# Optimization experiments

Hardware: AMD Instinct MI355X
Metric: run time of the kernel (lower is better)

## Reference

```python
import jax, jax.numpy as jnp
import numpy as np

DIM = 1024
NUM_HEADS = 16
HEAD_DIM = DIM // NUM_HEADS
ROPE_BASE = 10000.0


def _rope_cache(seq_len, head_dim, dtype=jnp.float32):
    inv_freq = 1.0 / (ROPE_BASE ** (jnp.arange(0, head_dim, 2, dtype=jnp.float32) / head_dim))
    t = jnp.arange(seq_len, dtype=jnp.float32)
    freqs = jnp.einsum('i,j->ij', t, inv_freq)          # [S, hd/2]
    emb = jnp.concatenate([freqs, freqs], axis=-1)       # [S, hd]
    return jnp.cos(emb).astype(dtype), jnp.sin(emb).astype(dtype)


def _rotate_half(x):
    x1, x2 = jnp.split(x, 2, axis=-1)
    return jnp.concatenate([-x2, x1], axis=-1)


def setup_inputs() -> dict:
    key = jax.random.key(0)
    k1, k2, k3 = jax.random.split(key, 3)
    B, S, D = 2, 2048, DIM
    x = jax.random.normal(k1, (B, S, D), dtype=jnp.float32)
    mask = jnp.tril(jnp.ones((S, S), dtype=jnp.bool_))   # causal mask
    w_qkv = jax.random.normal(k2, (D, 3 * D), dtype=jnp.float32) * (D ** -0.5)
    w_out = jax.random.normal(k3, (D, D), dtype=jnp.float32) * (D ** -0.5)
    return {"x": x, "w_qkv": w_qkv, "w_out": w_out, "mask": mask}


def reference(x, w_qkv, w_out, mask):
    B, S, D = x.shape
    H, hd = NUM_HEADS, HEAD_DIM
    qkv = x @ w_qkv                                       # [B,S,3D]
    q, k, v = jnp.split(qkv, 3, axis=-1)
    # [B,H,S,hd]
    q = q.reshape(B, S, H, hd).transpose(0, 2, 1, 3)
    k = k.reshape(B, S, H, hd).transpose(0, 2, 1, 3)
    v = v.reshape(B, S, H, hd).transpose(0, 2, 1, 3)
    cos, sin = _rope_cache(S, hd, q.dtype)               # [S,hd]
    q = q * cos + _rotate_half(q) * sin
    k = k * cos + _rotate_half(k) * sin
    scale = hd ** -0.5
    scores = jnp.einsum('bhqd,bhkd->bhqk', q, k) * scale  # [B,H,S,S]
    neg = jnp.finfo(scores.dtype).min
    scores = jnp.where(mask[None, None, :, :], scores, neg)
    attn = jax.nn.softmax(scores, axis=-1)                # dropout off (eval)
    out = jnp.einsum('bhqk,bhkd->bhqd', attn, v)
    out = out.transpose(0, 2, 1, 3).reshape(B, S, D)
    return out @ w_out
```

## Files before the change

kernel.cpp:

```cpp
#include <hip/hip_runtime.h>

typedef __attribute__((ext_vector_type(8))) short short8;
typedef __attribute__((ext_vector_type(4))) float f32x4;
typedef __attribute__((ext_vector_type(16))) float f32x16;

__device__ __forceinline__ unsigned short f2bf(float f) {
    unsigned u = __builtin_bit_cast(unsigned, f);
    u += 0x7FFFu + ((u >> 16) & 1u);
    return (unsigned short)(u >> 16);
}
__device__ __forceinline__ short8 ld_frag(const uint4* p, size_t idx16) {
    return __builtin_bit_cast(short8, p[idx16]);
}
__device__ __forceinline__ unsigned cvt_pk_bf16(float lo, float hi) {
    unsigned r;
    asm("v_cvt_pk_bf16_f32 %0, %1, %2" : "=v"(r) : "v"(lo), "v"(hi));
    return r;
}
__device__ __forceinline__ void gload_lds16(const void* g, void* l) {
    __builtin_amdgcn_global_load_lds((const __attribute__((address_space(1))) void*)g,
                                     (__attribute__((address_space(3))) void*)l, 16, 0, 0);
}

__global__ __launch_bounds__(256) void prep_kernel(const float* __restrict__ x, unsigned short* __restrict__ xb,
                                                   const float* __restrict__ wqkv, unsigned short* __restrict__ wqkvT,
                                                   const float* __restrict__ wout, unsigned short* __restrict__ woutT,
                                                   float* __restrict__ cosT, float* __restrict__ sinT) {
    __shared__ float t[32][33];
    int bid = blockIdx.x, tid = threadIdx.x;
    if (bid < 256) {
        int idx = bid * 256 + tid;
        int s = idx >> 5, i = idx & 31;
        float inv = powf(10000.f, -(float)i / 32.f);
        float ang = (float)s * inv;
        cosT[idx] = cosf(ang);
        sinT[idx] = sinf(ang);
        return;
    }
    if (bid < 4352) {
        int i = (bid - 256) * 256 + tid;
        float4 v = reinterpret_cast<const float4*>(x)[i];
        ushort4 o;
        o.x = f2bf(v.x); o.y = f2bf(v.y); o.z = f2bf(v.z); o.w = f2bf(v.w);
        reinterpret_cast<ushort4*>(xb)[i] = o;
        return;
    }
    const float* in; unsigned short* out; int R, C, c0, r0;
    if (bid < 7424) {
        int b2 = bid - 4352;
        in = wqkv; out = wqkvT; R = 1024; C = 3072;
        c0 = (b2 % 96) * 32; r0 = (b2 / 96) * 32;
    } else {
        int b2 = bid - 7424;
        in = wout; out = woutT; R = 1024; C = 1024;
        c0 = (b2 % 32) * 32; r0 = (b2 / 32) * 32;
    }
    int tx = tid & 31, ty = tid >> 5;
    for (int i = 0; i < 4; ++i)
        t[ty + i * 8][tx] = in[(size_t)(r0 + ty + i * 8) * C + c0 + tx];
    __syncthreads();
    for (int i = 0; i < 4; ++i)
        out[(size_t)(c0 + ty + i * 8) * R + r0 + tx] = f2bf(t[tx][ty + i * 8]);
}

template <bool OUT_BF16, int NF>
__global__ __launch_bounds__(256) void gemm_bt_kernel(const unsigned short* __restrict__ A,
                                                      const unsigned short* __restrict__ Bt,
                                                      void* __restrict__ Cout,
                                                      int M, int N, int K) {
    constexpr int BN = NF * 32;
    __shared__ __align__(16) unsigned short As[2][128 * 32];
    __shared__ __align__(16) unsigned short Bs[2][BN * 32];
    int tid = threadIdx.x;
    int lane = tid & 63;
    int w = tid >> 6;
    int wm = w >> 1, wn = w & 1;
    int m0 = blockIdx.y * 128, n0 = blockIdx.x * BN;
    int rq = lane >> 4, cl = lane & 15;

    f32x4 acc[4][NF] = {};
    const uint4* As4 = reinterpret_cast<const uint4*>(As);
    const uint4* Bs4 = reinterpret_cast<const uint4*>(Bs);

    #pragma unroll
    for (int i = 0; i < 2; ++i) {
        int c = i * 256 + tid;
        int r = c >> 2, cc = c & 3;
        gload_lds16(A + (size_t)(m0 + r) * K + cc * 8,
                    (char*)As[0] + (size_t)(i * 256 + w * 64) * 16);
    }
    #pragma unroll
    for (int i = 0; i < NF / 2; ++i) {
        int c = i * 256 + tid;
        int r = c >> 2, cc = c & 3;
        gload_lds16(Bt + (size_t)(n0 + r) * K + cc * 8,
                    (char*)Bs[0] + (size_t)(i * 256 + w * 64) * 16);
    }
    __syncthreads();
    int cur = 0;

    for (int k0 = 0; k0 < K; k0 += 32) {
        short8 af[4], bfr[NF];
        #pragma unroll
        for (int mf = 0; mf < 4; ++mf) {
            int row = wm * 64 + mf * 16 + cl;
            af[mf] = ld_frag(As4, cur * 512 + row * 4 + rq);
        }
        #pragma unroll
        for (int nf = 0; nf < NF; ++nf) {
            int row = wn * (NF * 16) + nf * 16 + cl;
            bfr[nf] = ld_frag(Bs4, cur * (NF * 128) + row * 4 + rq);
        }
        if (k0 + 32 < K) {
            int kn = k0 + 32;
            #pragma unroll
            for (int i = 0; i < 2; ++i) {
                int c = i * 256 + tid;
                int r = c >> 2, cc = c & 3;
                gload_lds16(A + (size_t)(m0 + r) * K + kn + cc * 8,
                            (char*)As[cur ^ 1] + (size_t)(i * 256 + w * 64) * 16);
            }
            #pragma unroll
            for (int i = 0; i < NF / 2; ++i) {
                int c = i * 256 + tid;
                int r = c >> 2, cc = c & 3;
                gload_lds16(Bt + (size_t)(n0 + r) * K + kn + cc * 8,
                            (char*)Bs[cur ^ 1] + (size_t)(i * 256 + w * 64) * 16);
            }
        }
        __builtin_amdgcn_s_setprio(1);
        #pragma unroll
        for (int mf = 0; mf < 4; ++mf)
            #pragma unroll
            for (int nf = 0; nf < NF; ++nf)
                acc[mf][nf] = __builtin_amdgcn_mfma_f32_16x16x32_bf16(af[mf], bfr[nf], acc[mf][nf], 0, 0, 0);
        __builtin_amdgcn_s_setprio(0);
        __syncthreads();
        cur ^= 1;
    }
    #pragma unroll
    for (int mf = 0; mf < 4; ++mf)
        #pragma unroll
        for (int nf = 0; nf < NF; ++nf)
            #pragma unroll
            for (int r = 0; r < 4; ++r) {
                size_t row = m0 + wm * 64 + mf * 16 + rq * 4 + r;
                size_t col = n0 + wn * (NF * 16) + nf * 16 + cl;
                float v = acc[mf][nf][r];
                if (OUT_BF16)
                    ((unsigned short*)Cout)[row * N + col] = f2bf(v);
                else
                    ((float*)Cout)[row * N + col] = v;
            }
}

__global__ __launch_bounds__(256) void gemm_qkv_rope_kernel(const unsigned short* __restrict__ A,
                                                            const unsigned short* __restrict__ Bt,
                                                            const float* __restrict__ cosT,
                                                            const float* __restrict__ sinT,
                                                            unsigned short* __restrict__ Qb,
                                                            unsigned short* __restrict__ Kb,
                                                            unsigned short* __restrict__ VT) {
    const int K = 1024;
    __shared__ __align__(16) unsigned short As[2][128 * 32];
    __shared__ __align__(16) unsigned short Bs[2][128 * 32];
    int tid = threadIdx.x;
    int lane = tid & 63;
    int w = tid >> 6;
    int wm = w >> 1, wn = w & 1;
    int m0 = blockIdx.y * 128, n0 = blockIdx.x * 128;
    int rq = lane >> 4, cl = lane & 15;

    f32x4 acc[4][4] = {};
    const uint4* As4 = reinterpret_cast<const uint4*>(As);
    const uint4* Bs4 = reinterpret_cast<const uint4*>(Bs);

    #pragma unroll
    for (int i = 0; i < 2; ++i) {
        int c = i * 256 + tid;
        int r = c >> 2, cc = c & 3;
        gload_lds16(A + (size_t)(m0 + r) * K + cc * 8,
                    (char*)As[0] + (size_t)(i * 256 + w * 64) * 16);
        gload_lds16(Bt + (size_t)(n0 + r) * K + cc * 8,
                    (char*)Bs[0] + (size_t)(i * 256 + w * 64) * 16);
    }
    __syncthreads();
    int cur = 0;

    for (int k0 = 0; k0 < K; k0 += 32) {
        short8 af[4], bfr[4];
        #pragma unroll
        for (int mf = 0; mf < 4; ++mf)
            af[mf] = ld_frag(As4, cur * 512 + (wm * 64 + mf * 16 + cl) * 4 + rq);
        #pragma unroll
        for (int nf = 0; nf < 4; ++nf)
            bfr[nf] = ld_frag(Bs4, cur * 512 + (wn * 64 + nf * 16 + cl) * 4 + rq);
        if (k0 + 32 < K) {
            int kn = k0 + 32;
            #pragma unroll
            for (int i = 0; i < 2; ++i) {
                int c = i * 256 + tid;
                int r = c >> 2, cc = c & 3;
                gload_lds16(A + (size_t)(m0 + r) * K + kn + cc * 8,
                            (char*)As[cur ^ 1] + (size_t)(i * 256 + w * 64) * 16);
                gload_lds16(Bt + (size_t)(n0 + r) * K + kn + cc * 8,
                            (char*)Bs[cur ^ 1] + (size_t)(i * 256 + w * 64) * 16);
            }
        }
        __builtin_amdgcn_s_setprio(1);
        #pragma unroll
        for (int mf = 0; mf < 4; ++mf)
            #pragma unroll
            for (int nf = 0; nf < 4; ++nf)
                acc[mf][nf] = __builtin_amdgcn_mfma_f32_16x16x32_bf16(af[mf], bfr[nf], acc[mf][nf], 0, 0, 0);
        __builtin_amdgcn_s_setprio(0);
        __syncthreads();
        cur ^= 1;
    }

    const float QSCALE = 0.125f * 1.44269504088896f;
    int colbase = n0 + wn * 64;
    int sect = colbase >> 10;
    int h = (colbase >> 6) & 15;
    #pragma unroll
    for (int mf = 0; mf < 4; ++mf) {
        int row0 = m0 + wm * 64 + mf * 16 + rq * 4;
        int b = row0 >> 11;
        int s0r = row0 & 2047;
        size_t ho = (size_t)(b * 16 + h);
        if (sect == 2) {
            #pragma unroll
            for (int nf = 0; nf < 4; ++nf) {
                int d = nf * 16 + cl;
                ushort4 o;
                o.x = f2bf(acc[mf][nf][0]);
                o.y = f2bf(acc[mf][nf][1]);
                o.z = f2bf(acc[mf][nf][2]);
                o.w = f2bf(acc[mf][nf][3]);
                *reinterpret_cast<ushort4*>(VT + (ho * 64 + d) * 2048 + s0r) = o;
            }
        } else {
            unsigned short* dst = (sect == 0) ? Qb : Kb;
            float scale = (sect == 0) ? QSCALE : 1.0f;
            #pragma unroll
            for (int nf = 0; nf < 4; ++nf) {
                int d = nf * 16 + cl;
                int f = ((nf & 1) << 4) + cl;
                #pragma unroll
                for (int r = 0; r < 4; ++r) {
                    int s = s0r + r;
                    float cs = cosT[s * 32 + f], sn = sinT[s * 32 + f];
                    float val = acc[mf][nf][r], pair = acc[mf][nf ^ 2][r];
                    float out = (nf < 2) ? val * cs - pair * sn : val * cs + pair * sn;
                    dst[(ho * 2048 + s) * 64 + d] = f2bf(out * scale);
                }
            }
        }
    }
}

__global__ __launch_bounds__(512) void flash_attn_kernel(const unsigned short* __restrict__ Qb,
                                                         const unsigned short* __restrict__ Kb,
                                                         const unsigned short* __restrict__ VT,
                                                         unsigned short* __restrict__ Oattn) {
    const int S = 2048;
    __shared__ __align__(16) char smem[65536 + 512];
    int tid = threadIdx.x, lane = tid & 63, w = tid >> 6;
    int qsub = w & 1, kvh = (w >> 1) & 1, st = w >> 2;
    int gid = blockIdx.x;
    int hh = gid & 31;
    int cp = gid >> 5;
    size_t headOff = (size_t)hh * S * 64;
    const unsigned short* Kg = Kb + headOff;
    const unsigned short* Vg = VT + headOff;
    const uint4* Qg4 = reinterpret_cast<const uint4*>(Qb + headOff);
    int l31 = lane & 31, hi = lane >> 5;

    int sr = tid >> 3;
    int sj = ((tid & 7) ^ (sr & 7)) * 8;
    char* Kst = smem + st * 16384;
    char* Vst = smem + 32768 + st * 16384;
    float* mo = reinterpret_cast<float*>(smem);
    float* ml = reinterpret_cast<float*>(smem + 49152);

    #pragma unroll
    for (int ph = 0; ph < 2; ++ph) {
        int c = ph ? (31 - cp) : cp;
        int q0 = c * 64;
        int qw = q0 + qsub * 32;
        int qrow = qw + l31;
        int nk = c + 1;
        int nr = (nk + 1) >> 1;

        short8 qf[4];
        #pragma unroll
        for (int cc = 0; cc < 4; ++cc)
            qf[cc] = ld_frag(Qg4, (size_t)qrow * 8 + cc * 2 + hi);

        f32x16 oacc0 = {}, oacc1 = {};
        float l = 0.f;

        gload_lds16(Kg + (0 * 64 + sr) * 64 + sj, smem + 0 * 16384 + tid * 16);
        gload_lds16(Vg + (size_t)sr * S + 0 * 64 + sj, smem + 32768 + 0 * 16384 + tid * 16);
        if (nk > 1) {
            gload_lds16(Kg + (1 * 64 + sr) * 64 + sj, smem + 1 * 16384 + tid * 16);
            gload_lds16(Vg + (size_t)sr * S + 1 * 64 + sj, smem + 32768 + 1 * 16384 + tid * 16);
        }
        __syncthreads();
        int cur = 0;

        for (int rd = 0; rd < nr; ++rd) {
            int kt = 2 * rd + st;
            int kvbase = kt * 64 + kvh * 32;
            bool active = (kt < nk) && (kvbase <= qw + 31);
            short8 ka[4], va[4];
            if (active) {
                const char* Kt = Kst + cur * 8192;
                const char* Vt = Vst + cur * 8192;
                int r = kvh * 32 + l31;
                #pragma unroll
                for (int cc = 0; cc < 4; ++cc)
                    ka[cc] = __builtin_bit_cast(short8, *reinterpret_cast<const uint4*>(
                        Kt + r * 128 + (((2 * cc + hi) ^ (r & 7)) * 16)));
                #pragma unroll
                for (int t = 0; t < 2; ++t) {
                    va[t] = __builtin_bit_cast(short8, *reinterpret_cast<const uint4*>(
                        Vt + l31 * 128 + (((kvh * 4 + 2 * t + hi) ^ (l31 & 7)) * 16)));
                    va[2 + t] = __builtin_bit_cast(short8, *reinterpret_cast<const uint4*>(
                        Vt + (32 + l31) * 128 + (((kvh * 4 + 2 * t + hi) ^ ((32 + l31) & 7)) * 16)));
                }
            }
            {
                int kt2 = 2 * rd + 2;
                if (kt2 < nk) {
                    gload_lds16(Kg + (kt2 * 64 + sr) * 64 + sj,
                                smem + 0 * 16384 + (cur ^ 1) * 8192 + tid * 16);
                    gload_lds16(Vg + (size_t)sr * S + kt2 * 64 + sj,
                                smem + 32768 + 0 * 16384 + (cur ^ 1) * 8192 + tid * 16);
                }
                if (kt2 + 1 < nk) {
                    gload_lds16(Kg + ((kt2 + 1) * 64 + sr) * 64 + sj,
                                smem + 1 * 16384 + (cur ^ 1) * 8192 + tid * 16);
                    gload_lds16(Vg + (size_t)sr * S + (kt2 + 1) * 64 + sj,
                                smem + 32768 + 1 * 16384 + (cur ^ 1) * 8192 + tid * 16);
                }
            }
            if (active) {
                f32x16 s = {};
                __builtin_amdgcn_s_setprio(1);
                #pragma unroll
                for (int cc = 0; cc < 4; ++cc)
                    s = __builtin_amdgcn_mfma_f32_32x32x16_bf16(ka[cc], qf[cc], s, 0, 0, 0);
                __builtin_amdgcn_s_setprio(0);

                if (kvbase + 31 > qw) {
                    #pragma unroll
                    for (int r = 0; r < 16; ++r) {
                        int kva = kvbase + (r & 3) + 8 * (r >> 2) + 4 * hi;
                        s[r] = (kva <= qrow) ? s[r] : -1e30f;
                    }
                }
                #pragma unroll
                for (int r = 0; r < 16; ++r) s[r] = exp2f(s[r]);
                float rp0 = ((s[0] + s[4]) + (s[8] + s[12])) + ((s[1] + s[5]) + (s[9] + s[13]));
                float rp1 = ((s[2] + s[6]) + (s[10] + s[14])) + ((s[3] + s[7]) + (s[11] + s[15]));
                float rs = rp0 + rp1;
                rs += __shfl_xor(rs, 32);
                l += rs;

                unsigned wd[8];
                #pragma unroll
                for (int i = 0; i < 8; ++i) wd[i] = cvt_pk_bf16(s[2 * i], s[2 * i + 1]);
                unsigned e0 = (unsigned)__shfl_xor((int)(hi ? wd[0] : wd[2]), 32);
                unsigned e1 = (unsigned)__shfl_xor((int)(hi ? wd[1] : wd[3]), 32);
                unsigned e2 = (unsigned)__shfl_xor((int)(hi ? wd[4] : wd[6]), 32);
                unsigned e3 = (unsigned)__shfl_xor((int)(hi ? wd[5] : wd[7]), 32);
                uint4 p0 = hi ? uint4{e0, e1, wd[2], wd[3]} : uint4{wd[0], wd[1], e0, e1};
                uint4 p1 = hi ? uint4{e2, e3, wd[6], wd[7]} : uint4{wd[4], wd[5], e2, e3};
                short8 pb0 = __builtin_bit_cast(short8, p0);
                short8 pb1 = __builtin_bit_cast(short8, p1);

                __builtin_amdgcn_s_setprio(1);
                oacc0 = __builtin_amdgcn_mfma_f32_32x32x16_bf16(va[0], pb0, oacc0, 0, 0, 0);
                oacc0 = __builtin_amdgcn_mfma_f32_32x32x16_bf16(va[1], pb1, oacc0, 0, 0, 0);
                oacc1 = __builtin_amdgcn_mfma_f32_32x32x16_bf16(va[2], pb0, oacc1, 0, 0, 0);
                oacc1 = __builtin_amdgcn_mfma_f32_32x32x16_bf16(va[3], pb1, oacc1, 0, 0, 0);
                __builtin_amdgcn_s_setprio(0);
            }
            __syncthreads();
            cur ^= 1;
        }

        int pub = (kvh << 1 | st) - 1;
        if (pub >= 0) {
            #pragma unroll
            for (int r = 0; r < 16; ++r) {
                mo[((pub * 32 + r) * 2 + qsub) * 64 + lane]      = oacc0[r];
                mo[((pub * 32 + 16 + r) * 2 + qsub) * 64 + lane] = oacc1[r];
            }
            ml[(pub * 2 + qsub) * 64 + lane] = l;
        }
        __syncthreads();
        if (pub < 0) {
            #pragma unroll
            for (int p = 0; p < 3; ++p) {
                l += ml[(p * 2 + qsub) * 64 + lane];
                #pragma unroll
                for (int r = 0; r < 16; ++r) {
                    oacc0[r] += mo[((p * 32 + r) * 2 + qsub) * 64 + lane];
                    oacc1[r] += mo[((p * 32 + 16 + r) * 2 + qsub) * 64 + lane];
                }
            }
            float invl = 1.f / l;
            size_t orow = ((size_t)((hh >> 4) * 2048 + qrow)) * 1024 + (hh & 15) * 64;
            #pragma unroll
            for (int du = 0; du < 2; ++du) {
                const f32x16& oa = du ? oacc1 : oacc0;
                #pragma unroll
                for (int gq = 0; gq < 4; ++gq) {
                    ushort4 o;
                    #pragma unroll
                    for (int e = 0; e < 4; ++e)
                        ((unsigned short*)&o)[e] = f2bf(oa[4 * gq + e] * invl);
                    int d = du * 32 + 4 * hi + 8 * gq;
                    *reinterpret_cast<ushort4*>(Oattn + orow + d) = o;
                }
            }
        }
        __syncthreads();
    }
}

extern "C" void kernel_launch(void* const* d_in, const int* in_sizes, int n_in,
                              void* d_out, int out_size, void* d_ws, size_t ws_size,
                              hipStream_t stream) {
    const float* x    = (const float*)d_in[0];
    const float* wqkv = (const float*)d_in[1];
    const float* wout = (const float*)d_in[2];

    char* ws = (char*)d_ws;
    unsigned short* xb    = (unsigned short*)(ws);
    unsigned short* wqkvT = (unsigned short*)(ws + (8ull  << 20));
    unsigned short* woutT = (unsigned short*)(ws + (14ull << 20));
    unsigned short* Qb    = (unsigned short*)(ws + (40ull << 20));
    unsigned short* Kb    = (unsigned short*)(ws + (48ull << 20));
    unsigned short* VT    = (unsigned short*)(ws + (56ull << 20));
    unsigned short* Oat   = (unsigned short*)(ws + (64ull << 20));
    float* cosT           = (float*)(ws + (72ull << 20));
    float* sinT           = (float*)(ws + (72ull << 20) + (256u << 10));

    prep_kernel<<<8448, 256, 0, stream>>>(x, xb, wqkv, wqkvT, wout, woutT, cosT, sinT);
    gemm_qkv_rope_kernel<<<dim3(24, 32), 256, 0, stream>>>(xb, wqkvT, cosT, sinT, Qb, Kb, VT);
    flash_attn_kernel<<<512, 512, 0, stream>>>(Qb, Kb, VT, Oat);
    gemm_bt_kernel<false, 2><<<dim3(16, 32), 256, 0, stream>>>(Oat, woutT, d_out, 4096, 1024, 1024);
}
```

Before: 115.3 us.

## Restructure flash attention to per-wave private KV staging without block barriers

The attention block shrinks from 8 to 4 waves. Each wave now streams its own 32-row K/V slice into a private double-buffered LDS region, using vmcnt waits instead of block-wide __syncthreads in the inner loop. Per-wave trip counts skip fully masked causal tiles, and the cross-wave reduction falls from four partial sums to two. This removes barrier stalls and idle waves in the causal loop, but halves the threads per block and gives up the shared K/V reuse across waves.

Measured after the change: 116.6 us. No clear change (+1.1%).

```diff
diff --git a/kernel.cpp b/kernel.cpp
--- a/kernel.cpp
+++ b/kernel.cpp
@@ -259,14 +259,14 @@
     }
 }
 
-__global__ __launch_bounds__(512) void flash_attn_kernel(const unsigned short* __restrict__ Qb,
+__global__ __launch_bounds__(256) void flash_attn_kernel(const unsigned short* __restrict__ Qb,
                                                          const unsigned short* __restrict__ Kb,
                                                          const unsigned short* __restrict__ VT,
                                                          unsigned short* __restrict__ Oattn) {
     const int S = 2048;
-    __shared__ __align__(16) char smem[65536 + 512];
+    __shared__ __align__(16) char smem[65536];
     int tid = threadIdx.x, lane = tid & 63, w = tid >> 6;
-    int qsub = w & 1, kvh = (w >> 1) & 1, st = w >> 2;
+    int qsub = w & 1, kvh = w >> 1;
     int gid = blockIdx.x;
     int hh = gid & 31;
     int cp = gid >> 5;
@@ -276,12 +276,12 @@
     const uint4* Qg4 = reinterpret_cast<const uint4*>(Qb + headOff);
     int l31 = lane & 31, hi = lane >> 5;
 
-    int sr = tid >> 3;
-    int sj = ((tid & 7) ^ (sr & 7)) * 8;
-    char* Kst = smem + st * 16384;
-    char* Vst = smem + 32768 + st * 16384;
+    char* my = smem + w * 16384;
+    int r8 = lane >> 3, c8 = lane & 7;
+    int r4 = lane >> 2, c4 = lane & 3;
+    int svl = (l31 ^ (l31 >> 2)) & 3;
     float* mo = reinterpret_cast<float*>(smem);
-    float* ml = reinterpret_cast<float*>(smem + 49152);
+    float* ml = reinterpret_cast<float*>(smem + 32768);
 
     #pragma unroll
     for (int ph = 0; ph < 2; ++ph) {
@@ -290,127 +290,119 @@
         int qw = q0 + qsub * 32;
         int qrow = qw + l31;
         int nk = c + 1;
-        int nr = (nk + 1) >> 1;
+        int lim = qw + 31 - 32 * kvh;
+        int nkw = (lim >= 0) ? (lim >> 6) + 1 : 0;
+        if (nkw > nk) nkw = nk;
 
         short8 qf[4];
         #pragma unroll
         for (int cc = 0; cc < 4; ++cc)
             qf[cc] = ld_frag(Qg4, (size_t)qrow * 8 + cc * 2 + hi);
+        asm volatile("s_waitcnt vmcnt(0)" ::: "memory");
 
         f32x16 oacc0 = {}, oacc1 = {};
         float l = 0.f;
 
-        gload_lds16(Kg + (0 * 64 + sr) * 64 + sj, smem + 0 * 16384 + tid * 16);
-        gload_lds16(Vg + (size_t)sr * S + 0 * 64 + sj, smem + 32768 + 0 * 16384 + tid * 16);
-        if (nk > 1) {
-            gload_lds16(Kg + (1 * 64 + sr) * 64 + sj, smem + 1 * 16384 + tid * 16);
-            gload_lds16(Vg + (size_t)sr * S + 1 * 64 + sj, smem + 32768 + 1 * 16384 + tid * 16);
-        }
-        __syncthreads();
-        int cur = 0;
-
-        for (int rd = 0; rd < nr; ++rd) {
-            int kt = 2 * rd + st;
+        auto stage = [&](int kt, int b) {
+            char* kb = my + b * 8192;
+            char* vb = my + b * 8192 + 4096;
+            int kvb = kt * 64 + kvh * 32;
+            #pragma unroll
+            for (int j = 0; j < 4; ++j)
+                gload_lds16(Kg + (size_t)(kvb + 8 * j + r8) * 64 + ((c8 ^ (r8 & 7)) * 8),
+                            kb + j * 1024);
+            #pragma unroll
+            for (int j = 0; j < 4; ++j) {
+                int d = 16 * j + r4;
+                int sv = (d ^ (d >> 2)) & 3;
+                gload_lds16(Vg + (size_t)d * S + kvb + ((c4 ^ sv) * 8),
+                            vb + j * 1024);
+            }
+        };
+
+        if (nkw > 0) stage(0, 0);
+        for (int kt = 0; kt < nkw; ++kt) {
+            int b = kt & 1;
+            if (kt + 1 < nkw) {
+                stage(kt + 1, b ^ 1);
+                asm volatile("s_waitcnt vmcnt(8)" ::: "memory");
+            } else {
+                asm volatile("s_waitcnt vmcnt(0)" ::: "memory");
+            }
+            __builtin_amdgcn_sched_barrier(0);
+            const char* kb = my + b * 8192;
+            const char* vb = my + b * 8192 + 4096;
             int kvbase = kt * 64 + kvh * 32;
-            bool active = (kt < nk) && (kvbase <= qw + 31);
+
             short8 ka[4], va[4];
-            if (active) {
-                const char* Kt = Kst + cur * 8192;
-                const char* Vt = Vst + cur * 8192;
-                int r = kvh * 32 + l31;
-                #pragma unroll
-                for (int cc = 0; cc < 4; ++cc)
-                    ka[cc] = __builtin_bit_cast(short8, *reinterpret_cast<const uint4*>(
-                        Kt + r * 128 + (((2 * cc + hi) ^ (r & 7)) * 16)));
-                #pragma unroll
-                for (int t = 0; t < 2; ++t) {
-                    va[t] = __builtin_bit_cast(short8, *reinterpret_cast<const uint4*>(
-                        Vt + l31 * 128 + (((kvh * 4 + 2 * t + hi) ^ (l31 & 7)) * 16)));
-                    va[2 + t] = __builtin_bit_cast(short8, *reinterpret_cast<const uint4*>(
-                        Vt + (32 + l31) * 128 + (((kvh * 4 + 2 * t + hi) ^ ((32 + l31) & 7)) * 16)));
-                }
-            }
-            {
-                int kt2 = 2 * rd + 2;
-                if (kt2 < nk) {
-                    gload_lds16(Kg + (kt2 * 64 + sr) * 64 + sj,
-                                smem + 0 * 16384 + (cur ^ 1) * 8192 + tid * 16);
-                    gload_lds16(Vg + (size_t)sr * S + kt2 * 64 + sj,
-                                smem + 32768 + 0 * 16384 + (cur ^ 1) * 8192 + tid * 16);
-                }
-                if (kt2 + 1 < nk) {
-                    gload_lds16(Kg + ((kt2 + 1) * 64 + sr) * 64 + sj,
-                                smem + 1 * 16384 + (cur ^ 1) * 8192 + tid * 16);
-                    gload_lds16(Vg + (size_t)sr * S + (kt2 + 1) * 64 + sj,
-                                smem + 32768 + 1 * 16384 + (cur ^ 1) * 8192 + tid * 16);
-                }
-            }
-            if (active) {
-                f32x16 s = {};
-                __builtin_amdgcn_s_setprio(1);
-                #pragma unroll
-                for (int cc = 0; cc < 4; ++cc)
-                    s = __builtin_amdgcn_mfma_f32_32x32x16_bf16(ka[cc], qf[cc], s, 0, 0, 0);
-                __builtin_amdgcn_s_setprio(0);
-
-                if (kvbase + 31 > qw) {
-                    #pragma unroll
-                    for (int r = 0; r < 16; ++r) {
-                        int kva = kvbase + (r & 3) + 8 * (r >> 2) + 4 * hi;
-                        s[r] = (kva <= qrow) ? s[r] : -1e30f;
-                    }
-                }
-                #pragma unroll
-                for (int r = 0; r < 16; ++r) s[r] = exp2f(s[r]);
-                float rp0 = ((s[0] + s[4]) + (s[8] + s[12])) + ((s[1] + s[5]) + (s[9] + s[13]));
-                float rp1 = ((s[2] + s[6]) + (s[10] + s[14])) + ((s[3] + s[7]) + (s[11] + s[15]));
-                float rs = rp0 + rp1;
-                rs += __shfl_xor(rs, 32);
-                l += rs;
-
-                unsigned wd[8];
-                #pragma unroll
-                for (int i = 0; i < 8; ++i) wd[i] = cvt_pk_bf16(s[2 * i], s[2 * i + 1]);
-                unsigned e0 = (unsigned)__shfl_xor((int)(hi ? wd[0] : wd[2]), 32);
-                unsigned e1 = (unsigned)__shfl_xor((int)(hi ? wd[1] : wd[3]), 32);
-                unsigned e2 = (unsigned)__shfl_xor((int)(hi ? wd[4] : wd[6]), 32);
-                unsigned e3 = (unsigned)__shfl_xor((int)(hi ? wd[5] : wd[7]), 32);
-                uint4 p0 = hi ? uint4{e0, e1, wd[2], wd[3]} : uint4{wd[0], wd[1], e0, e1};
-                uint4 p1 = hi ? uint4{e2, e3, wd[6], wd[7]} : uint4{wd[4], wd[5], e2, e3};
-                short8 pb0 = __builtin_bit_cast(short8, p0);
-                short8 pb1 = __builtin_bit_cast(short8, p1);
-
-                __builtin_amdgcn_s_setprio(1);
-                oacc0 = __builtin_amdgcn_mfma_f32_32x32x16_bf16(va[0], pb0, oacc0, 0, 0, 0);
-                oacc0 = __builtin_amdgcn_mfma_f32_32x32x16_bf16(va[1], pb1, oacc0, 0, 0, 0);
-                oacc1 = __builtin_amdgcn_mfma_f32_32x32x16_bf16(va[2], pb0, oacc1, 0, 0, 0);
-                oacc1 = __builtin_amdgcn_mfma_f32_32x32x16_bf16(va[3], pb1, oacc1, 0, 0, 0);
-                __builtin_amdgcn_s_setprio(0);
-            }
-            __syncthreads();
-            cur ^= 1;
-        }
-
-        int pub = (kvh << 1 | st) - 1;
-        if (pub >= 0) {
-            #pragma unroll
-            for (int r = 0; r < 16; ++r) {
-                mo[((pub * 32 + r) * 2 + qsub) * 64 + lane]      = oacc0[r];
-                mo[((pub * 32 + 16 + r) * 2 + qsub) * 64 + lane] = oacc1[r];
-            }
-            ml[(pub * 2 + qsub) * 64 + lane] = l;
-        }
-        __syncthreads();
-        if (pub < 0) {
-            #pragma unroll
-            for (int p = 0; p < 3; ++p) {
-                l += ml[(p * 2 + qsub) * 64 + lane];
+            #pragma unroll
+            for (int cc = 0; cc < 4; ++cc)
+                ka[cc] = __builtin_bit_cast(short8, *reinterpret_cast<const uint4*>(
+                    kb + l31 * 128 + (((2 * cc + hi) ^ (l31 & 7)) * 16)));
+            #pragma unroll
+            for (int t = 0; t < 2; ++t) {
+                va[t] = __builtin_bit_cast(short8, *reinterpret_cast<const uint4*>(
+                    vb + l31 * 64 + (((2 * t + hi) ^ svl) * 16)));
+                va[2 + t] = __builtin_bit_cast(short8, *reinterpret_cast<const uint4*>(
+                    vb + (32 + l31) * 64 + (((2 * t + hi) ^ svl) * 16)));
+            }
+
+            f32x16 s = {};
+            __builtin_amdgcn_s_setprio(1);
+            #pragma unroll
+            for (int cc = 0; cc < 4; ++cc)
+                s = __builtin_amdgcn_mfma_f32_32x32x16_bf16(ka[cc], qf[cc], s, 0, 0, 0);
+            __builtin_amdgcn_s_setprio(0);
+
+            if (kvbase + 31 > qw) {
                 #pragma unroll
                 for (int r = 0; r < 16; ++r) {
-                    oacc0[r] += mo[((p * 32 + r) * 2 + qsub) * 64 + lane];
-                    oacc1[r] += mo[((p * 32 + 16 + r) * 2 + qsub) * 64 + lane];
+                    int kva = kvbase + (r & 3) + 8 * (r >> 2) + 4 * hi;
+                    s[r] = (kva <= qrow) ? s[r] : -1e30f;
                 }
             }
+            #pragma unroll
+            for (int r = 0; r < 16; ++r) s[r] = exp2f(s[r]);
+            float rp0 = ((s[0] + s[4]) + (s[8] + s[12])) + ((s[1] + s[5]) + (s[9] + s[13]));
+            float rp1 = ((s[2] + s[6]) + (s[10] + s[14])) + ((s[3] + s[7]) + (s[11] + s[15]));
+            float rs = rp0 + rp1;
+            rs += __shfl_xor(rs, 32);
+            l += rs;
+
+            unsigned wd[8];
+            #pragma unroll
+            for (int i = 0; i < 8; ++i) wd[i] = cvt_pk_bf16(s[2 * i], s[2 * i + 1]);
+            unsigned e0 = (unsigned)__shfl_xor((int)(hi ? wd[0] : wd[2]), 32);
+            unsigned e1 = (unsigned)__shfl_xor((int)(hi ? wd[1] : wd[3]), 32);
+            unsigned e2 = (unsigned)__shfl_xor((int)(hi ? wd[4] : wd[6]), 32);
+            unsigned e3 = (unsigned)__shfl_xor((int)(hi ? wd[5] : wd[7]), 32);
+            uint4 p0 = hi ? uint4{e0, e1, wd[2], wd[3]} : uint4{wd[0], wd[1], e0, e1};
+            uint4 p1 = hi ? uint4{e2, e3, wd[6], wd[7]} : uint4{wd[4], wd[5], e2, e3};
+            short8 pb0 = __builtin_bit_cast(short8, p0);
+            short8 pb1 = __builtin_bit_cast(short8, p1);
+
+            __builtin_amdgcn_s_setprio(1);
+            oacc0 = __builtin_amdgcn_mfma_f32_32x32x16_bf16(va[0], pb0, oacc0, 0, 0, 0);
+            oacc0 = __builtin_amdgcn_mfma_f32_32x32x16_bf16(va[1], pb1, oacc0, 0, 0, 0);
+            oacc1 = __builtin_amdgcn_mfma_f32_32x32x16_bf16(va[2], pb0, oacc1, 0, 0, 0);
+            oacc1 = __builtin_amdgcn_mfma_f32_32x32x16_bf16(va[3], pb1, oacc1, 0, 0, 0);
+            __builtin_amdgcn_s_setprio(0);
+        }
+
+        asm volatile("s_waitcnt vmcnt(0)" ::: "memory");
+        __syncthreads();
+
+        if (kvh) {
+            #pragma unroll
+            for (int r = 0; r < 16; ++r) {
+                mo[(r * 2 + qsub) * 64 + lane]        = oacc0[r];
+                mo[((16 + r) * 2 + qsub) * 64 + lane] = oacc1[r];
+            }
+            ml[qsub * 64 + lane] = l;
+        }
+        __syncthreads();
+        if (!kvh) {
+            l += ml[qsub * 64 + lane];
             float invl = 1.f / l;
             size_t orow = ((size_t)((hh >> 4) * 2048 + qrow)) * 1024 + (hh & 15) * 64;
             #pragma unroll
@@ -420,8 +412,10 @@
                 for (int gq = 0; gq < 4; ++gq) {
                     ushort4 o;
                     #pragma unroll
-                    for (int e = 0; e < 4; ++e)
-                        ((unsigned short*)&o)[e] = f2bf(oa[4 * gq + e] * invl);
+                    for (int e = 0; e < 4; ++e) {
+                        int r = 4 * gq + e;
+                        ((unsigned short*)&o)[e] = f2bf((oa[r] + mo[((du * 16 + r) * 2 + qsub) * 64 + lane]) * invl);
+                    }
                     int d = du * 32 + 4 * hi + 8 * gq;
                     *reinterpret_cast<ushort4*>(Oattn + orow + d) = o;
                 }
@@ -451,6 +445,6 @@
 
     prep_kernel<<<8448, 256, 0, stream>>>(x, xb, wqkv, wqkvT, wout, woutT, cosT, sinT);
     gemm_qkv_rope_kernel<<<dim3(24, 32), 256, 0, stream>>>(xb, wqkvT, cosT, sinT, Qb, Kb, VT);
-    flash_attn_kernel<<<512, 512, 0, stream>>>(Qb, Kb, VT, Oat);
+    flash_attn_kernel<<<512, 256, 0, stream>>>(Qb, Kb, VT, Oat);
     gemm_bt_kernel<false, 2><<<dim3(16, 32), 256, 0, stream>>>(Oat, woutT, d_out, 4096, 1024, 1024);
 }
```
